# Performance work log

Measured on AMD Instinct MI355X. Metric: run time of the kernel, lower is better.

## Reference

```python
import jax, jax.numpy as jnp
import numpy as np


def _conv1x1(x, w, b):
    # x: (B, C, H, W), w: (O, C), b: (O,) -> (B, O, H, W)
    return jnp.einsum('bchw,oc->bohw', x, w) + b[None, :, None, None]


def setup_inputs() -> dict:
    key = jax.random.key(0)
    ks = jax.random.split(key, 9)
    C, Cb = 256, 128
    B, H, W = 4, 64, 64
    s_in = 1.0 / np.sqrt(C)   # kaiming-uniform-ish scale for 1x1 convs
    s_bn = 1.0 / np.sqrt(Cb)
    return {
        'x': jax.random.normal(ks[0], (B, C, H, W), dtype=jnp.float32),
        'theta_w': jax.random.uniform(ks[1], (Cb, C), jnp.float32, -s_in, s_in),
        'theta_b': jax.random.uniform(ks[2], (Cb,), jnp.float32, -s_in, s_in),
        'phi_w': jax.random.uniform(ks[3], (Cb, C), jnp.float32, -s_in, s_in),
        'phi_b': jax.random.uniform(ks[4], (Cb,), jnp.float32, -s_in, s_in),
        'g_w': jax.random.uniform(ks[5], (Cb, C), jnp.float32, -s_in, s_in),
        'g_b': jax.random.uniform(ks[6], (Cb,), jnp.float32, -s_in, s_in),
        'W_w': jax.random.uniform(ks[7], (C, Cb), jnp.float32, -s_bn, s_bn),
        'W_b': jax.random.uniform(ks[8], (C,), jnp.float32, -s_bn, s_bn),
    }


def reference(x, theta_w, theta_b, phi_w, phi_b, g_w, g_b, W_w, W_b):
    B, C, H, Wd = x.shape
    Cb = theta_w.shape[0]
    # NOTE: the original uses raw torch.reshape (row-major), NOT transpose,
    # so (B, Cb, H, W) -> (B, H*W, Cb) scrambles channel/spatial layout.
    # We replicate that exactly with jnp.reshape.
    theta = _conv1x1(x, theta_w, theta_b).reshape(B, -1, Cb)   # (B, N, Cb)
    phi = _conv1x1(x, phi_w, phi_b).reshape(B, Cb, -1)         # (B, Cb, N)
    g = _conv1x1(x, g_w, g_b).reshape(B, -1, Cb)               # (B, N, Cb)
    scores = jnp.einsum('bnc,bcm->bnm', theta, phi)            # (B, N, N)
    attn = jax.nn.softmax(scores, axis=1)                      # softmax over dim=1 (unusual axis)
    y = jnp.einsum('bnm,bmc->bnc', attn, g)                    # (B, N, Cb)
    y = y.reshape(B, -1, H, Wd)                                # raw reshape back to (B, Cb, H, W)
    w = _conv1x1(y, W_w, W_b)                                  # (B, C, H, W)
    return w + x
```

## Files before the change

### kernel.cpp

```cpp
#include <hip/hip_runtime.h>
#include <math.h>

constexpr int CI = 256;
constexpr int CB = 128;
constexpr int HWD = 4096;
constexpr int NBATCH = 4;
constexpr int NN_ = 4096;
constexpr size_t U1 = (size_t)NBATCH * NN_ * CB;
constexpr size_t U_THETA = 0;
constexpr size_t U_PHIT  = U1;
constexpr size_t U_G     = 2 * U1;
constexpr size_t U_GT    = 3 * U1;
constexpr size_t U_Y     = 4 * U1;
constexpr size_t U_XT    = 4 * U1;
constexpr size_t U_WCAT  = 8 * U1;
constexpr size_t U_WW    = 8 * U1 + 98304;
constexpr size_t F_D     = (8 * U1 + 131072) / 2;

typedef short v8s __attribute__((ext_vector_type(8)));
typedef unsigned short u8s __attribute__((ext_vector_type(8)));
typedef float v4f __attribute__((ext_vector_type(4)));
typedef float v16f __attribute__((ext_vector_type(16)));
#define MFMA16(a, b, c) __builtin_amdgcn_mfma_f32_16x16x32_bf16(a, b, c, 0, 0, 0)
#define MFMA32(a, b, c) __builtin_amdgcn_mfma_f32_32x32x16_bf16(a, b, c, 0, 0, 0)

__device__ __forceinline__ unsigned short f2bf(float f) {
    union { float f; unsigned u; } v; v.f = f;
    unsigned r = v.u + 0x7fff + ((v.u >> 16) & 1);
    return (unsigned short)(r >> 16);
}
__device__ __forceinline__ float bf2f(unsigned short s) {
    union { unsigned u; float f; } v; v.u = (unsigned)s << 16;
    return v.f;
}

__global__ __launch_bounds__(256) void k0_xpose(
    const float* __restrict__ x, unsigned short* __restrict__ xT)
{
    __shared__ unsigned short T[64 * 72];
    const int t = threadIdx.x;
    const int hw0 = blockIdx.x * 64, c0 = blockIdx.y * 64, b = blockIdx.z;
    const float* xb = x + (size_t)b * CI * HWD;
    const int rr = t >> 4, cc = t & 15;
    #pragma unroll
    for (int pass = 0; pass < 4; pass++) {
        float4 f = *(const float4*)&xb[(size_t)(c0 + pass * 16 + rr) * HWD + hw0 + cc * 4];
        T[(cc * 4 + 0) * 72 + pass * 16 + rr] = f2bf(f.x);
        T[(cc * 4 + 1) * 72 + pass * 16 + rr] = f2bf(f.y);
        T[(cc * 4 + 2) * 72 + pass * 16 + rr] = f2bf(f.z);
        T[(cc * 4 + 3) * 72 + pass * 16 + rr] = f2bf(f.w);
    }
    __syncthreads();
    const int row = t >> 2, cs = (t & 3) * 16;
    unsigned short* dst = xT + (size_t)b * NN_ * CI;
    #pragma unroll
    for (int h = 0; h < 2; h++)
        *(u8s*)&dst[(size_t)(hw0 + row) * CI + c0 + cs + h * 8] =
            *(const u8s*)&T[row * 72 + cs + h * 8];
}

__global__ __launch_bounds__(256) void k0_weights(
    const float* __restrict__ tw, const float* __restrict__ pw,
    const float* __restrict__ gw, const float* __restrict__ Ww,
    unsigned short* __restrict__ wcat, unsigned short* __restrict__ wwB)
{
    int e = (blockIdx.x * 256 + threadIdx.x) * 4;
    const float* src; unsigned short* dst;
    if (e < 32768)       { src = tw + e;          dst = wcat + e; }
    else if (e < 65536)  { src = pw + (e - 32768); dst = wcat + e; }
    else if (e < 98304)  { src = gw + (e - 65536); dst = wcat + e; }
    else                 { src = Ww + (e - 98304); dst = wwB + (e - 98304); }
    float4 f = *(const float4*)src;
    ushort4 u;
    u.x = f2bf(f.x); u.y = f2bf(f.y); u.z = f2bf(f.z); u.w = f2bf(f.w);
    *(ushort4*)dst = u;
}

__global__ __launch_bounds__(256, 4) void k1_mfma(
    const unsigned short* __restrict__ xT, const unsigned short* __restrict__ wcat,
    const float* __restrict__ tb, const float* __restrict__ pb,
    const float* __restrict__ gb,
    unsigned short* __restrict__ thetaB, unsigned short* __restrict__ phiTB,
    unsigned short* __restrict__ gB)
{
    __shared__ unsigned short LdsX[64 * 268];
    unsigned short* T = LdsX;
    const int t = threadIdx.x;
    const int lane = t & 63, w = t >> 6;
    const int l31 = lane & 31, lh = lane >> 5;
    const int qj = w >> 1, qh = w & 1;
    const int hw0 = blockIdx.x * 64, j0 = blockIdx.y * 64, b = blockIdx.z;
    const int matId = j0 >> 7, jl0 = j0 & 127;
    const float* bvec = (matId == 0) ? tb : (matId == 1) ? pb : gb;
    const unsigned short* xb = xT + (size_t)b * NN_ * CI;

    {
        const int row = t >> 2, seg = t & 3;
        #pragma unroll
        for (int c8 = 0; c8 < 8; c8++)
            *(u8s*)&LdsX[row * 268 + seg * 64 + c8 * 8] =
                *(const u8s*)&xb[(size_t)(hw0 + row) * CI + seg * 64 + c8 * 8];
    }
    __syncthreads();

    v16f s = {};
    #pragma unroll
    for (int kt = 0; kt < 16; kt++) {
        v8s a = *(const v8s*)&wcat[(size_t)(j0 + qj * 32 + l31) * CI + kt * 16 + lh * 8];
        v8s bx = *(const v8s*)&LdsX[(qh * 32 + l31) * 268 + kt * 16 + lh * 8];
        s = MFMA32(a, bx, s);
    }

    if (matId != 1) {
        unsigned short* dst = ((matId == 0) ? thetaB : gB) + (size_t)b * CB * HWD;
        #pragma unroll
        for (int reg = 0; reg < 16; reg++) {
            int row = (reg & 3) + 8 * (reg >> 2) + 4 * lh;
            int cb = jl0 + qj * 32 + row;
            dst[(size_t)cb * HWD + hw0 + qh * 32 + l31] = f2bf(s[reg] + bvec[cb]);
        }
    } else {
        __syncthreads();
        #pragma unroll
        for (int reg = 0; reg < 16; reg++) {
            int row = (reg & 3) + 8 * (reg >> 2) + 4 * lh;
            T[(qh * 32 + l31) * 76 + qj * 32 + row] =
                f2bf(s[reg] + bvec[jl0 + qj * 32 + row]);
        }
        __syncthreads();
        unsigned short* dst = phiTB + (size_t)b * NN_ * CB;
        const int row = t >> 2, cs = (t & 3) * 16;
        #pragma unroll
        for (int h = 0; h < 2; h++)
            *(u8s*)&dst[(size_t)(hw0 + row) * CB + jl0 + cs + h * 8] =
                *(const u8s*)&T[row * 76 + cs + h * 8];
    }
}

__global__ __launch_bounds__(256, 4) void k2_colsum(
    const unsigned short* __restrict__ thetaB,
    const unsigned short* __restrict__ phiTB,
    float* __restrict__ Dout)
{
    __shared__ float part[4][64];
    const int t = threadIdx.x;
    const int lane = t & 63, w = t >> 6;
    const int ln = lane & 15, quad = lane >> 4;
    const int m0 = blockIdx.x * 64, q = blockIdx.y, b = blockIdx.z;
    const unsigned short* th = thetaB + (size_t)b * NN_ * CB;
    const unsigned short* ph = phiTB + (size_t)b * NN_ * CB;

    v8s bf[4][4];
    #pragma unroll
    for (int mt = 0; mt < 4; mt++)
        #pragma unroll
        for (int kt = 0; kt < 4; kt++)
            bf[mt][kt] = *(const v8s*)&ph[(size_t)(m0 + mt * 16 + ln) * CB + kt * 32 + quad * 8];

    float dsum[4] = {0.f, 0.f, 0.f, 0.f};
    const int nBeg = q * 1024 + w * 16, nEnd = q * 1024 + 1024;
    v8s af[4], afn[4];
    #pragma unroll
    for (int kt = 0; kt < 4; kt++)
        af[kt] = *(const v8s*)&th[(size_t)(nBeg + ln) * CB + kt * 32 + quad * 8];
    for (int n0 = nBeg; n0 < nEnd; n0 += 64) {
        int nn = (n0 + 64 < nEnd) ? n0 + 64 : nBeg;
        #pragma unroll
        for (int kt = 0; kt < 4; kt++)
            afn[kt] = *(const v8s*)&th[(size_t)(nn + ln) * CB + kt * 32 + quad * 8];
        v4f s[4] = {};
        #pragma unroll
        for (int mt = 0; mt < 4; mt++)
            #pragma unroll
            for (int kt = 0; kt < 4; kt++)
                s[mt] = MFMA16(af[kt], bf[mt][kt], s[mt]);
        #pragma unroll
        for (int mt = 0; mt < 4; mt++)
            #pragma unroll
            for (int r = 0; r < 4; r++)
                dsum[mt] += __expf(s[mt][r]);
        #pragma unroll
        for (int kt = 0; kt < 4; kt++) af[kt] = afn[kt];
    }
    #pragma unroll
    for (int mt = 0; mt < 4; mt++) {
        float v = dsum[mt];
        v += __shfl_xor(v, 16);
        v += __shfl_xor(v, 32);
        dsum[mt] = v;
    }
    if (quad == 0) {
        #pragma unroll
        for (int mt = 0; mt < 4; mt++) part[w][mt * 16 + ln] = dsum[mt];
    }
    __syncthreads();
    if (t < 64) {
        float v = part[0][t] + part[1][t] + part[2][t] + part[3][t];
        Dout[((size_t)q * NBATCH + b) * NN_ + m0 + t] = v;
    }
}

__global__ __launch_bounds__(256) void k1b_transpose_scale_g(
    const unsigned short* __restrict__ gB, const float* __restrict__ D,
    unsigned short* __restrict__ gTB)
{
    __shared__ unsigned short T[128 * 36];
    const int t = threadIdx.x;
    const int m0 = blockIdx.x * 32;
    const int b  = blockIdx.z;
    const unsigned short* F = gB + (size_t)b * CB * HWD;
    unsigned short* dst = gTB + (size_t)b * CB * HWD;
    const int mrow = t >> 3, cg = t & 7;
    {
        int m = m0 + mrow;
        float d = D[((size_t)0 * NBATCH + b) * NN_ + m]
                + D[((size_t)1 * NBATCH + b) * NN_ + m]
                + D[((size_t)2 * NBATCH + b) * NN_ + m]
                + D[((size_t)3 * NBATCH + b) * NN_ + m];
        float r = 1.0f / d;
        #pragma unroll
        for (int j8 = 0; j8 < 2; j8++) {
            int cbase = cg * 8 + j8 * 64;
            u8s u = *(const u8s*)&F[(size_t)m * CB + cbase];
            #pragma unroll
            for (int e = 0; e < 8; e++)
                T[(cbase + e) * 36 + mrow] = f2bf(bf2f(u[e]) * r);
        }
    }
    __syncthreads();
    const int c = t >> 1, mh = (t & 1) * 16;
    #pragma unroll
    for (int h8 = 0; h8 < 2; h8++)
        *(u8s*)&dst[(size_t)c * HWD + m0 + mh + h8 * 8] =
            *(const u8s*)&T[c * 36 + mh + h8 * 8];
}

__global__ __launch_bounds__(256, 4) void k3_attn(
    const unsigned short* __restrict__ thetaB,
    const unsigned short* __restrict__ phiTB,
    const unsigned short* __restrict__ gTB,
    unsigned short* __restrict__ Y)
{
    __shared__ unsigned short Lphi[64 * 140];
    __shared__ unsigned short Pl[64 * 76];
    const int t = threadIdx.x;
    const int lane = t & 63, w = t >> 6;
    const int l31 = lane & 31, lh = lane >> 5;
    const int qn = w & 1, qm = w >> 1;
    const int rowS = t >> 4, colS = t & 15;
    const int n0 = blockIdx.x * 64, q = blockIdx.y, b = blockIdx.z;
    const unsigned short* th = thetaB + (size_t)b * NN_ * CB;
    const unsigned short* ph = phiTB + (size_t)b * NN_ * CB;
    const unsigned short* gT = gTB + (size_t)b * CB * HWD;

    v8s ath[8];
    #pragma unroll
    for (int kt = 0; kt < 8; kt++)
        ath[kt] = *(const v8s*)&th[(size_t)(n0 + qn * 32 + l31) * CB + kt * 16 + lh * 8];

    const int mBeg = q * 1024, mEnd = mBeg + 1024;
    #pragma unroll
    for (int pass = 0; pass < 4; pass++)
        *(v8s*)&Lphi[(pass * 16 + rowS) * 140 + colS * 8] =
            *(const v8s*)&ph[(size_t)(mBeg + pass * 16 + rowS) * CB + colS * 8];
    __syncthreads();

    v16f yacc[2] = {};
    for (int m0 = mBeg; m0 < mEnd; m0 += 64) {
        int mN = (m0 + 64 < mEnd) ? m0 + 64 : mBeg;
        v8s preg[4];
        #pragma unroll
        for (int pass = 0; pass < 4; pass++)
            preg[pass] = *(const v8s*)&ph[(size_t)(mN + pass * 16 + rowS) * CB + colS * 8];
        v16f s = {};
        #pragma unroll
        for (int kt = 0; kt < 8; kt++) {
            v8s bphi = *(const v8s*)&Lphi[(qm * 32 + l31) * 140 + kt * 16 + lh * 8];
            s = MFMA32(ath[kt], bphi, s);
        }
        __syncthreads();
        #pragma unroll
        for (int reg = 0; reg < 16; reg++) {
            int row = qn * 32 + (reg & 3) + 8 * (reg >> 2) + 4 * lh;
            Pl[row * 76 + qm * 32 + l31] = f2bf(__expf(s[reg]));
        }
        #pragma unroll
        for (int pass = 0; pass < 4; pass++)
            *(v8s*)&Lphi[(pass * 16 + rowS) * 140 + colS * 8] = preg[pass];
        __syncthreads();
        #pragma unroll
        for (int kstep = 0; kstep < 4; kstep++) {
            v8s bg = *(const v8s*)&gT[(size_t)(w * 32 + l31) * HWD + m0 + kstep * 16 + lh * 8];
            #pragma unroll
            for (int nt = 0; nt < 2; nt++) {
                v8s ap = *(const v8s*)&Pl[(nt * 32 + l31) * 76 + kstep * 16 + lh * 8];
                yacc[nt] = MFMA32(ap, bg, yacc[nt]);
            }
        }
    }
    unsigned short* yp = Y + ((size_t)q * NBATCH + b) * CB * HWD;
    #pragma unroll
    for (int nt = 0; nt < 2; nt++)
        #pragma unroll
        for (int reg = 0; reg < 16; reg++) {
            int row = (reg & 3) + 8 * (reg >> 2) + 4 * lh;
            yp[(size_t)(n0 + nt * 32 + row) * CB + w * 32 + l31] = f2bf(yacc[nt][reg]);
        }
}

__global__ __launch_bounds__(256, 2) void k4_mfma(
    const float* __restrict__ x, const unsigned short* __restrict__ wwB,
    const float* __restrict__ Wb, const unsigned short* __restrict__ Ybuf,
    float* __restrict__ out)
{
    __shared__ unsigned short Yt[64 * 136];
    const int t = threadIdx.x;
    const int lane = t & 63, w = t >> 6;
    const int ln = lane & 15, quad = lane >> 4;
    const int hw0 = blockIdx.x * 64, o0 = blockIdx.y * 128, b = blockIdx.z;

    const int cb = t >> 1, seg = (t & 1) * 32;
    #pragma unroll
    for (int g8 = 0; g8 < 4; g8++) {
        float sum[8] = {};
        #pragma unroll
        for (int q = 0; q < 4; q++) {
            u8s u = *(const u8s*)&Ybuf[((size_t)q * NBATCH + b) * CB * HWD +
                                       (size_t)cb * HWD + hw0 + seg + g8 * 8];
            #pragma unroll
            for (int j = 0; j < 8; j++) sum[j] += bf2f(u[j]);
        }
        #pragma unroll
        for (int j = 0; j < 8; j++)
            Yt[(seg + g8 * 8 + j) * 136 + cb] = f2bf(sum[j]);
    }
    __syncthreads();

    v8s aw[2][4];
    #pragma unroll
    for (int os = 0; os < 2; os++)
        #pragma unroll
        for (int kt = 0; kt < 4; kt++)
            aw[os][kt] = *(const v8s*)&wwB[(size_t)(o0 + w * 32 + os * 16 + ln) * CB + kt * 32 + quad * 8];

    v4f s[2][4] = {};
    #pragma unroll
    for (int kt = 0; kt < 4; kt++) {
        v8s by[4];
        #pragma unroll
        for (int mt = 0; mt < 4; mt++)
            by[mt] = *(const v8s*)&Yt[(mt * 16 + ln) * 136 + kt * 32 + quad * 8];
        #pragma unroll
        for (int os = 0; os < 2; os++)
            #pragma unroll
            for (int mt = 0; mt < 4; mt++)
                s[os][mt] = MFMA16(aw[os][kt], by[mt], s[os][mt]);
    }
    #pragma unroll
    for (int os = 0; os < 2; os++)
        #pragma unroll
        for (int mt = 0; mt < 4; mt++)
            #pragma unroll
            for (int r = 0; r < 4; r++) {
                int o = o0 + w * 32 + os * 16 + quad * 4 + r;
                size_t idx = (size_t)b * CI * HWD + (size_t)o * HWD + hw0 + mt * 16 + ln;
                out[idx] = s[os][mt][r] + Wb[o] + x[idx];
            }
}

extern "C" void kernel_launch(void* const* d_in, const int* in_sizes, int n_in,
                              void* d_out, int out_size, void* d_ws, size_t ws_size,
                              hipStream_t stream)
{
    const float* x  = (const float*)d_in[0];
    const float* tw = (const float*)d_in[1];
    const float* tb = (const float*)d_in[2];
    const float* pw = (const float*)d_in[3];
    const float* pb = (const float*)d_in[4];
    const float* gw = (const float*)d_in[5];
    const float* gb = (const float*)d_in[6];
    const float* Ww = (const float*)d_in[7];
    const float* Wb = (const float*)d_in[8];
    unsigned short* wsu = (unsigned short*)d_ws;
    float* wsf = (float*)d_ws;
    unsigned short* thetaB = wsu + U_THETA;
    unsigned short* phiTB  = wsu + U_PHIT;
    unsigned short* gB     = wsu + U_G;
    unsigned short* gTB    = wsu + U_GT;
    unsigned short* Ybuf   = wsu + U_Y;
    unsigned short* xTB    = wsu + U_XT;
    unsigned short* wcatB  = wsu + U_WCAT;
    unsigned short* wwB    = wsu + U_WW;
    float* Dbuf = wsf + F_D;
    float* out = (float*)d_out;
    dim3 blk(256, 1, 1);
    hipLaunchKernelGGL(k0_xpose, dim3(64, 4, NBATCH), blk, 0, stream, x, xTB);
    hipLaunchKernelGGL(k0_weights, dim3(128, 1, 1), blk, 0, stream,
                       tw, pw, gw, Ww, wcatB, wwB);
    hipLaunchKernelGGL(k1_mfma, dim3(64, 6, NBATCH), blk, 0, stream,
                       xTB, wcatB, tb, pb, gb, thetaB, phiTB, gB);
    hipLaunchKernelGGL(k2_colsum, dim3(64, 4, NBATCH), blk, 0, stream,
                       thetaB, phiTB, Dbuf);
    hipLaunchKernelGGL(k1b_transpose_scale_g, dim3(128, 1, NBATCH), blk, 0, stream,
                       gB, Dbuf, gTB);
    hipLaunchKernelGGL(k3_attn, dim3(64, 4, NBATCH), blk, 0, stream,
                       thetaB, phiTB, gTB, Ybuf);
    hipLaunchKernelGGL(k4_mfma, dim3(64, 2, NBATCH), blk, 0, stream,
                       x, wwB, Wb, Ybuf, out);
}
```

Before: 211.0 us.

## Enlarge attention tile to 128 rows, read phi from global, fold weight cast into transpose

The attention kernel now processes 128 query rows per block instead of 64. Each wave holds two theta fragments and reuses each phi fragment for two MFMAs, which doubles the reuse of the g loads. The LDS staging and prefetch of phi are removed, so phi fragments are read directly from global or cache. This halves the grid, lowers the occupancy target, and raises register pressure. Separately, the weight-conversion kernel is folded into the transpose kernel as an extra grid slice to save one launch.

```diff
diff --git a/kernel.cpp b/kernel.cpp
--- a/kernel.cpp
+++ b/kernel.cpp
@@ -35,10 +35,29 @@
 }
 
 __global__ __launch_bounds__(256) void k0_xpose(
-    const float* __restrict__ x, unsigned short* __restrict__ xT)
+    const float* __restrict__ x, unsigned short* __restrict__ xT,
+    const float* __restrict__ tw, const float* __restrict__ pw,
+    const float* __restrict__ gw, const float* __restrict__ Ww,
+    unsigned short* __restrict__ wcat, unsigned short* __restrict__ wwB)
 {
     __shared__ unsigned short T[64 * 72];
     const int t = threadIdx.x;
+    if (blockIdx.y == 4) {
+        int wb = blockIdx.x + 64 * blockIdx.z;
+        if (t < 128) {
+            int e = (wb * 128 + t) * 4;
+            const float* src; unsigned short* dst;
+            if (e < 32768)       { src = tw + e;           dst = wcat + e; }
+            else if (e < 65536)  { src = pw + (e - 32768); dst = wcat + e; }
+            else if (e < 98304)  { src = gw + (e - 65536); dst = wcat + e; }
+            else                 { src = Ww + (e - 98304); dst = wwB + (e - 98304); }
+            float4 f = *(const float4*)src;
+            ushort4 u;
+            u.x = f2bf(f.x); u.y = f2bf(f.y); u.z = f2bf(f.z); u.w = f2bf(f.w);
+            *(ushort4*)dst = u;
+        }
+        return;
+    }
     const int hw0 = blockIdx.x * 64, c0 = blockIdx.y * 64, b = blockIdx.z;
     const float* xb = x + (size_t)b * CI * HWD;
     const int rr = t >> 4, cc = t & 15;
@@ -57,23 +76,6 @@
     for (int h = 0; h < 2; h++)
         *(u8s*)&dst[(size_t)(hw0 + row) * CI + c0 + cs + h * 8] =
             *(const u8s*)&T[row * 72 + cs + h * 8];
-}
-
-__global__ __launch_bounds__(256) void k0_weights(
-    const float* __restrict__ tw, const float* __restrict__ pw,
-    const float* __restrict__ gw, const float* __restrict__ Ww,
-    unsigned short* __restrict__ wcat, unsigned short* __restrict__ wwB)
-{
-    int e = (blockIdx.x * 256 + threadIdx.x) * 4;
-    const float* src; unsigned short* dst;
-    if (e < 32768)       { src = tw + e;          dst = wcat + e; }
-    else if (e < 65536)  { src = pw + (e - 32768); dst = wcat + e; }
-    else if (e < 98304)  { src = gw + (e - 65536); dst = wcat + e; }
-    else                 { src = Ww + (e - 98304); dst = wwB + (e - 98304); }
-    float4 f = *(const float4*)src;
-    ushort4 u;
-    u.x = f2bf(f.x); u.y = f2bf(f.y); u.z = f2bf(f.z); u.w = f2bf(f.w);
-    *(ushort4*)dst = u;
 }
 
 __global__ __launch_bounds__(256, 4) void k1_mfma(
@@ -235,64 +237,52 @@
             *(const u8s*)&T[c * 36 + mh + h8 * 8];
 }
 
-__global__ __launch_bounds__(256, 4) void k3_attn(
+__global__ __launch_bounds__(256, 2) void k3_attn(
     const unsigned short* __restrict__ thetaB,
     const unsigned short* __restrict__ phiTB,
     const unsigned short* __restrict__ gTB,
     unsigned short* __restrict__ Y)
 {
-    __shared__ unsigned short Lphi[64 * 140];
-    __shared__ unsigned short Pl[64 * 76];
+    __shared__ unsigned short Pl[128 * 76];
     const int t = threadIdx.x;
     const int lane = t & 63, w = t >> 6;
     const int l31 = lane & 31, lh = lane >> 5;
-    const int qn = w & 1, qm = w >> 1;
-    const int rowS = t >> 4, colS = t & 15;
-    const int n0 = blockIdx.x * 64, q = blockIdx.y, b = blockIdx.z;
+    const int qm = w & 1, qn2 = w >> 1;
+    const int n0 = blockIdx.x * 128, q = blockIdx.y, b = blockIdx.z;
     const unsigned short* th = thetaB + (size_t)b * NN_ * CB;
     const unsigned short* ph = phiTB + (size_t)b * NN_ * CB;
     const unsigned short* gT = gTB + (size_t)b * CB * HWD;
 
-    v8s ath[8];
-    #pragma unroll
-    for (int kt = 0; kt < 8; kt++)
-        ath[kt] = *(const v8s*)&th[(size_t)(n0 + qn * 32 + l31) * CB + kt * 16 + lh * 8];
+    v8s ath[2][8];
+    #pragma unroll
+    for (int s2 = 0; s2 < 2; s2++)
+        #pragma unroll
+        for (int kt = 0; kt < 8; kt++)
+            ath[s2][kt] = *(const v8s*)&th[(size_t)(n0 + qn2 * 64 + s2 * 32 + l31) * CB + kt * 16 + lh * 8];
 
     const int mBeg = q * 1024, mEnd = mBeg + 1024;
-    #pragma unroll
-    for (int pass = 0; pass < 4; pass++)
-        *(v8s*)&Lphi[(pass * 16 + rowS) * 140 + colS * 8] =
-            *(const v8s*)&ph[(size_t)(mBeg + pass * 16 + rowS) * CB + colS * 8];
-    __syncthreads();
-
-    v16f yacc[2] = {};
+    v16f yacc[4] = {};
     for (int m0 = mBeg; m0 < mEnd; m0 += 64) {
-        int mN = (m0 + 64 < mEnd) ? m0 + 64 : mBeg;
-        v8s preg[4];
-        #pragma unroll
-        for (int pass = 0; pass < 4; pass++)
-            preg[pass] = *(const v8s*)&ph[(size_t)(mN + pass * 16 + rowS) * CB + colS * 8];
-        v16f s = {};
+        v16f s0 = {}, s1 = {};
         #pragma unroll
         for (int kt = 0; kt < 8; kt++) {
-            v8s bphi = *(const v8s*)&Lphi[(qm * 32 + l31) * 140 + kt * 16 + lh * 8];
-            s = MFMA32(ath[kt], bphi, s);
+            v8s bphi = *(const v8s*)&ph[(size_t)(m0 + qm * 32 + l31) * CB + kt * 16 + lh * 8];
+            s0 = MFMA32(ath[0][kt], bphi, s0);
+            s1 = MFMA32(ath[1][kt], bphi, s1);
         }
         __syncthreads();
         #pragma unroll
         for (int reg = 0; reg < 16; reg++) {
-            int row = qn * 32 + (reg & 3) + 8 * (reg >> 2) + 4 * lh;
-            Pl[row * 76 + qm * 32 + l31] = f2bf(__expf(s[reg]));
-        }
-        #pragma unroll
-        for (int pass = 0; pass < 4; pass++)
-            *(v8s*)&Lphi[(pass * 16 + rowS) * 140 + colS * 8] = preg[pass];
+            int rbase = (reg & 3) + 8 * (reg >> 2) + 4 * lh;
+            Pl[(qn2 * 64 + rbase) * 76 + qm * 32 + l31] = f2bf(__expf(s0[reg]));
+            Pl[(qn2 * 64 + 32 + rbase) * 76 + qm * 32 + l31] = f2bf(__expf(s1[reg]));
+        }
         __syncthreads();
         #pragma unroll
         for (int kstep = 0; kstep < 4; kstep++) {
             v8s bg = *(const v8s*)&gT[(size_t)(w * 32 + l31) * HWD + m0 + kstep * 16 + lh * 8];
             #pragma unroll
-            for (int nt = 0; nt < 2; nt++) {
+            for (int nt = 0; nt < 4; nt++) {
                 v8s ap = *(const v8s*)&Pl[(nt * 32 + l31) * 76 + kstep * 16 + lh * 8];
                 yacc[nt] = MFMA32(ap, bg, yacc[nt]);
             }
@@ -300,7 +290,7 @@
     }
     unsigned short* yp = Y + ((size_t)q * NBATCH + b) * CB * HWD;
     #pragma unroll
-    for (int nt = 0; nt < 2; nt++)
+    for (int nt = 0; nt < 4; nt++)
         #pragma unroll
         for (int reg = 0; reg < 16; reg++) {
             int row = (reg & 3) + 8 * (reg >> 2) + 4 * lh;
@@ -394,16 +384,15 @@
     float* Dbuf = wsf + F_D;
     float* out = (float*)d_out;
     dim3 blk(256, 1, 1);
-    hipLaunchKernelGGL(k0_xpose, dim3(64, 4, NBATCH), blk, 0, stream, x, xTB);
-    hipLaunchKernelGGL(k0_weights, dim3(128, 1, 1), blk, 0, stream,
-                       tw, pw, gw, Ww, wcatB, wwB);
+    hipLaunchKernelGGL(k0_xpose, dim3(64, 5, NBATCH), blk, 0, stream,
+                       x, xTB, tw, pw, gw, Ww, wcatB, wwB);
     hipLaunchKernelGGL(k1_mfma, dim3(64, 6, NBATCH), blk, 0, stream,
                        xTB, wcatB, tb, pb, gb, thetaB, phiTB, gB);
     hipLaunchKernelGGL(k2_colsum, dim3(64, 4, NBATCH), blk, 0, stream,
                        thetaB, phiTB, Dbuf);
     hipLaunchKernelGGL(k1b_transpose_scale_g, dim3(128, 1, NBATCH), blk, 0, stream,
                        gB, Dbuf, gTB);
-    hipLaunchKernelGGL(k3_attn, dim3(64, 4, NBATCH), blk, 0, stream,
+    hipLaunchKernelGGL(k3_attn, dim3(32, 4, NBATCH), blk, 0, stream,
                        thetaB, phiTB, gTB, Ybuf);
     hipLaunchKernelGGL(k4_mfma, dim3(64, 2, NBATCH), blk, 0, stream,
                        x, wwB, Wb, Ybuf, out);
```

New measurement: 221.4 us. 4.9% more time.
